# Performance work log

Measured on AMD Instinct MI355X. Metric: run time of the kernel, lower is better.

Reference implementation:

```python
import jax, jax.numpy as jnp
import numpy as np

N = 11616          # IMDB total nodes (hard-coded slices in source)
NHID = 512
L = 4              # num_layers (encoder and decoder each)
E = 371712         # ~32 avg degree
SIZES = [4278, 2081, 5257]
FEATS = [3066, 2081, 5257]
GAMMA = 3.0


def setup_inputs() -> dict:
    key = jax.random.key(0)
    ks = jax.random.split(key, 24)
    s = 0.02
    d = {}
    d["X0"] = jax.random.normal(ks[0], (SIZES[0], FEATS[0]), jnp.float32)
    d["X1"] = jax.random.normal(ks[1], (SIZES[1], FEATS[1]), jnp.float32)
    d["X2"] = jax.random.normal(ks[2], (SIZES[2], FEATS[2]), jnp.float32)
    d["src"] = jax.random.randint(ks[3], (E,), 0, N)
    d["dst"] = jax.random.randint(ks[4], (E,), 0, N)
    d["edge_w"] = jax.random.uniform(ks[5], (E,), jnp.float32) / 32.0  # ~normalized adjacency values
    d["adj_full"] = (jax.random.uniform(ks[6], (N, N), jnp.float32) < 0.005).astype(jnp.float32)
    # input projections fc_list: feat_dim -> nhid
    for i in range(3):
        d[f"fc_W{i}"] = jax.random.normal(ks[7 + i], (FEATS[i], NHID), jnp.float32) * s
        d[f"fc_b{i}"] = jnp.zeros((NHID,), jnp.float32)
    # stacked GraphConvolution weights (encoder / decoder)
    d["enc_W"] = jax.random.normal(ks[10], (L, NHID, NHID), jnp.float32) * s
    d["enc_b"] = jnp.zeros((L, NHID), jnp.float32)
    d["dec_W"] = jax.random.normal(ks[11], (L, NHID, NHID), jnp.float32) * s
    d["dec_b"] = jnp.zeros((L, NHID), jnp.float32)
    # output projections fc_list2: nhid -> feat_dim
    for i in range(3):
        d[f"out_W{i}"] = jax.random.normal(ks[12 + i], (NHID, FEATS[i]), jnp.float32) * s
        d[f"out_b{i}"] = jnp.zeros((FEATS[i],), jnp.float32)
    return d


def reference(X0, X1, X2, edge_w, adj_full,
              fc_W0, fc_b0, fc_W1, fc_b1, fc_W2, fc_b2,
              enc_W, enc_b, dec_W, dec_b,
              out_W0, out_b0, out_W1, out_b1, out_W2, out_b2,
              src, dst):
    def spmm(h):  # sparse A @ h via edge list
        return jax.ops.segment_sum(h[src] * edge_w[:, None], dst, num_segments=N)

    # per-type input projection, concat over node types -> [N, NHID]
    x = jnp.concatenate([X0 @ fc_W0 + fc_b0,
                         X1 @ fc_W1 + fc_b1,
                         X2 @ fc_W2 + fc_b2], axis=0)

    # encoder then decoder; per source: relu+dropout only at layer 0 (L>1 branch),
    # residual add for layers i>0; dropout is identity in eval mode.
    for W, b in ((enc_W, enc_b), (dec_W, dec_b)):
        for i in range(L):
            h = spmm(x @ W[i]) + b[i]
            x = jax.nn.relu(h) if i == 0 else x + h

    # IMDB slices of final embedding
    e0, e1, e2 = x[:SIZES[0]], x[SIZES[0]:SIZES[0] + SIZES[1]], x[SIZES[0] + SIZES[1]:]
    r0 = e0 @ out_W0 + out_b0
    r1 = e1 @ out_W1 + out_b1
    r2 = e2 @ out_W2 + out_b2

    # emb_loss_fun2: BCE(sigmoid(x x^T), adj_full), mean. Stable form:
    z = x @ x.T  # [N, N]
    emb_loss = jnp.mean(adj_full * jax.nn.softplus(-z) + (1.0 - adj_full) * jax.nn.softplus(z))

    # recon_loss_fun2 on type-0 features (cosine-based, power gamma)
    rn = r0 / jnp.maximum(jnp.linalg.norm(r0, axis=-1, keepdims=True), 1e-12)
    fn = X0 / jnp.maximum(jnp.linalg.norm(X0, axis=1, keepdims=True), 1e-12)
    recon_loss = jnp.mean((1.0 - jnp.sum(rn * fn, axis=-1)) ** GAMMA)

    return (r0, r1, r2, emb_loss, recon_loss)
```

## Files before the change

### kernel.cpp

```cpp
#include <hip/hip_runtime.h>
#include <math.h>

#define N_NODES 11616
#define NROWPAD 11776
#define NHID    512
#define EDGES   371712
#define S0 4278
#define S1 2081
#define S2 5257
#define F0 3066
#define F1 2081
#define F2 5257
#define NBLK 91
#define FC_KS 4
#define WPR 363

typedef __attribute__((ext_vector_type(8))) short bf16x8;
typedef __attribute__((ext_vector_type(4))) float f32x4;

#define GL2LDS(g, l) __builtin_amdgcn_global_load_lds(                         \
    (const __attribute__((address_space(1))) unsigned int*)(g),                \
    (__attribute__((address_space(3))) unsigned int*)(l), 16, 0, 0)

__device__ __forceinline__ int slot_of(int row, int kg)
{
    return row * 4 + (kg ^ ((row >> 1) & 3));
}

__global__ void k_init(double* __restrict__ accum, int* __restrict__ indeg,
                       int* __restrict__ cursor)
{
    int i = blockIdx.x * blockDim.x + threadIdx.x;
    if (i < 2) accum[i] = 0.0;
    if (i < N_NODES) { indeg[i] = 0; cursor[i] = 0; }
}

__global__ void k_padzero(short* __restrict__ xh, short* __restrict__ xl)
{
    int i = blockIdx.x * blockDim.x + threadIdx.x;
    const int base  = N_NODES * NHID;
    const int total = (NROWPAD - N_NODES) * NHID;
    if (i < total) { xh[base + i] = 0; xl[base + i] = 0; }
}

__global__ void k_adjbits(const float* __restrict__ adj, unsigned* __restrict__ bits)
{
    const long i = (long)blockIdx.x * 256 + threadIdx.x;
    const long total = (long)N_NODES * WPR;
    if (i >= total) return;
    const int r = (int)(i / WPR);
    const int w = (int)(i % WPR);
    const float4* rp = reinterpret_cast<const float4*>(adj + (long)r * N_NODES + w * 32);
    unsigned m = 0;
    #pragma unroll
    for (int j4 = 0; j4 < 8; ++j4) {
        float4 v = rp[j4];
        int b = j4 * 4;
        m |= (v.x != 0.f) ? (1u << b)       : 0u;
        m |= (v.y != 0.f) ? (1u << (b + 1)) : 0u;
        m |= (v.z != 0.f) ? (1u << (b + 2)) : 0u;
        m |= (v.w != 0.f) ? (1u << (b + 3)) : 0u;
    }
    bits[i] = m;
}

__global__ void k_count(const int* __restrict__ dst, int* __restrict__ indeg)
{
    int e = blockIdx.x * blockDim.x + threadIdx.x;
    if (e < EDGES) atomicAdd(&indeg[dst[e]], 1);
}

__global__ void k_scan(const int* __restrict__ indeg, int* __restrict__ rowptr)
{
    __shared__ int part[256];
    const int t = threadIdx.x;
    const int chunk = (N_NODES + 255) / 256;
    const int base = t * chunk;
    int s = 0;
    for (int i = 0; i < chunk; ++i) {
        int idx = base + i;
        if (idx < N_NODES) s += indeg[idx];
    }
    part[t] = s;
    __syncthreads();
    if (t == 0) for (int i = 1; i < 256; ++i) part[i] += part[i - 1];
    __syncthreads();
    int run = (t == 0) ? 0 : part[t - 1];
    for (int i = 0; i < chunk; ++i) {
        int idx = base + i;
        if (idx < N_NODES) { rowptr[idx] = run; run += indeg[idx]; }
    }
    if (t == 0) rowptr[N_NODES] = part[255];
}

__global__ void k_fill(const int* __restrict__ src, const int* __restrict__ dst,
                       const float* __restrict__ ew, const int* __restrict__ rowptr,
                       int* __restrict__ cursor, int* __restrict__ csrc,
                       float* __restrict__ cw)
{
    int e = blockIdx.x * blockDim.x + threadIdx.x;
    if (e >= EDGES) return;
    int d = dst[e];
    int pos = rowptr[d] + atomicAdd(&cursor[d], 1);
    csrc[pos] = src[e];
    cw[pos]   = ew[e];
}

__device__ __forceinline__ void split_bf16(float f, short& hi, short& lo)
{
    unsigned u  = __float_as_uint(f);
    unsigned hr = (u + 0x7FFFu + ((u >> 16) & 1u)) & 0xFFFF0000u;
    float    fh = __uint_as_float(hr);
    float    fl = f - fh;
    unsigned ul = __float_as_uint(fl);
    unsigned lr = ul + 0x7FFFu + ((ul >> 16) & 1u);
    hi = (short)(hr >> 16);
    lo = (short)(lr >> 16);
}

__global__ void k_splitpad(const float* __restrict__ in, short* __restrict__ oh,
                           short* __restrict__ ol, int R, int C, int Cpad)
{
    const int c = blockIdx.x * 256 + threadIdx.x;
    const int r = blockIdx.y;
    if (c >= Cpad) return;
    float f = (r < R && c < C) ? in[(long)r * C + c] : 0.f;
    short h, l;
    split_bf16(f, h, l);
    oh[(long)r * Cpad + c] = h;
    ol[(long)r * Cpad + c] = l;
}

__global__ void k_tsplit(const float* __restrict__ in, short* __restrict__ oh,
                         short* __restrict__ ol, int R, int C, int Rpad, int Cpad)
{
    __shared__ float tile[32][33];
    const int cb = blockIdx.x * 32, rb = blockIdx.y * 32;
    const int tx = threadIdx.x, ty = threadIdx.y;
    #pragma unroll
    for (int i = ty; i < 32; i += 8) {
        int r = rb + i, c = cb + tx;
        tile[i][tx] = (r < R && c < C) ? in[(long)r * C + c] : 0.f;
    }
    __syncthreads();
    #pragma unroll
    for (int i = ty; i < 32; i += 8) {
        int row = cb + i, col = rb + tx;
        if (row < Cpad && col < Rpad) {
            short h, l;
            split_bf16(tile[tx][i], h, l);
            oh[(long)row * Rpad + col] = h;
            ol[(long)row * Rpad + col] = l;
        }
    }
}

__device__ __forceinline__ void stage_gl(const short* __restrict__ src, int ldk,
                                         int k0, short* ldsPanel, int lane)
{
    #pragma unroll
    for (int i = 0; i < 8; ++i) {
        int ci  = i * 64 + lane;
        int row = ci >> 2;
        int kgs = (ci & 3) ^ ((row >> 1) & 3);
        const short* g = src + (long)row * ldk + k0 + kgs * 8;
        GL2LDS(g, (char*)ldsPanel + i * 1024);
    }
}

__global__ __launch_bounds__(256, 3)
void k_gemm_bb(const short* __restrict__ Agh, const short* __restrict__ Agl,
               const short* __restrict__ Bgh, const short* __restrict__ Bgl,
               const float* __restrict__ bias, float* __restrict__ C,
               int M, int NN, int Kpad, int ldk)
{
    __shared__ short P[4][4096];
    const int t = threadIdx.x, lane = t & 63, w = t >> 6;
    const int rowBase = blockIdx.y * 128, colBase = blockIdx.x * 128;
    const int wm = (w >> 1) * 64, wn = (w & 1) * 64;
    const int kg = lane >> 4, fr = lane & 15;

    const short* srcs[4] = { Agh + (long)rowBase * ldk, Agl + (long)rowBase * ldk,
                             Bgh + (long)colBase * ldk, Bgl + (long)colBase * ldk };
    const short* mySrc = srcs[w];

    int offA[4], offB[4];
    #pragma unroll
    for (int f = 0; f < 4; ++f) {
        int rA = wm + f * 16 + fr, rB = wn + f * 16 + fr;
        offA[f] = slot_of(rA, kg) * 8;
        offB[f] = slot_of(rB, kg) * 8;
    }

    f32x4 acc[4][4];
    #pragma unroll
    for (int i = 0; i < 4; ++i)
        #pragma unroll
        for (int j = 0; j < 4; ++j)
            acc[i][j] = (f32x4){0.f, 0.f, 0.f, 0.f};

    for (int k0 = 0; k0 < Kpad; k0 += 32) {
        stage_gl(mySrc, ldk, k0, &P[w][0], lane);
        __syncthreads();
        bf16x8 ah[4], al[4], bh[4], bl[4];
        #pragma unroll
        for (int f = 0; f < 4; ++f) {
            ah[f] = *(const bf16x8*)&P[0][offA[f]];
            al[f] = *(const bf16x8*)&P[1][offA[f]];
            bh[f] = *(const bf16x8*)&P[2][offB[f]];
            bl[f] = *(const bf16x8*)&P[3][offB[f]];
        }
        #pragma unroll
        for (int i = 0; i < 4; ++i)
            #pragma unroll
            for (int j = 0; j < 4; ++j) {
                acc[i][j] = __builtin_amdgcn_mfma_f32_16x16x32_bf16(ah[i], bh[j], acc[i][j], 0, 0, 0);
                acc[i][j] = __builtin_amdgcn_mfma_f32_16x16x32_bf16(ah[i], bl[j], acc[i][j], 0, 0, 0);
                acc[i][j] = __builtin_amdgcn_mfma_f32_16x16x32_bf16(al[i], bh[j], acc[i][j], 0, 0, 0);
            }
        __syncthreads();
    }

    #pragma unroll
    for (int i = 0; i < 4; ++i) {
        #pragma unroll
        for (int q = 0; q < 4; ++q) {
            int r = rowBase + wm + i * 16 + kg * 4 + q;
            if (r >= M) continue;
            #pragma unroll
            for (int j = 0; j < 4; ++j) {
                int c = colBase + wn + j * 16 + fr;
                if (c < NN)
                    C[(long)r * NN + c] = acc[i][j][q] + (bias ? bias[c] : 0.f);
            }
        }
    }
}

__global__ __launch_bounds__(256, 3)
void k_gemm_red(const short* __restrict__ Agh, const short* __restrict__ Agl,
                const short* __restrict__ Bgh, const short* __restrict__ Bgl,
                float* __restrict__ Cpart, int M, int ldk, int kChunk)
{
    __shared__ short P[4][4096];
    const int t = threadIdx.x, lane = t & 63, w = t >> 6;
    const int rowBase = blockIdx.y * 128, colBase = blockIdx.x * 128;
    const int z = blockIdx.z;
    const int wm = (w >> 1) * 64, wn = (w & 1) * 64;
    const int kg = lane >> 4, fr = lane & 15;

    const short* srcs[4] = { Agh + (long)rowBase * ldk, Agl + (long)rowBase * ldk,
                             Bgh + (long)colBase * ldk, Bgl + (long)colBase * ldk };
    const short* mySrc = srcs[w];

    int offA[4], offB[4];
    #pragma unroll
    for (int f = 0; f < 4; ++f) {
        int rA = wm + f * 16 + fr, rB = wn + f * 16 + fr;
        offA[f] = slot_of(rA, kg) * 8;
        offB[f] = slot_of(rB, kg) * 8;
    }

    f32x4 acc[4][4];
    #pragma unroll
    for (int i = 0; i < 4; ++i)
        #pragma unroll
        for (int j = 0; j < 4; ++j)
            acc[i][j] = (f32x4){0.f, 0.f, 0.f, 0.f};

    const int kEnd = z * kChunk + kChunk;
    for (int k0 = z * kChunk; k0 < kEnd; k0 += 32) {
        stage_gl(mySrc, ldk, k0, &P[w][0], lane);
        __syncthreads();
        bf16x8 ah[4], al[4], bh[4], bl[4];
        #pragma unroll
        for (int f = 0; f < 4; ++f) {
            ah[f] = *(const bf16x8*)&P[0][offA[f]];
            al[f] = *(const bf16x8*)&P[1][offA[f]];
            bh[f] = *(const bf16x8*)&P[2][offB[f]];
            bl[f] = *(const bf16x8*)&P[3][offB[f]];
        }
        #pragma unroll
        for (int i = 0; i < 4; ++i)
            #pragma unroll
            for (int j = 0; j < 4; ++j) {
                acc[i][j] = __builtin_amdgcn_mfma_f32_16x16x32_bf16(ah[i], bh[j], acc[i][j], 0, 0, 0);
                acc[i][j] = __builtin_amdgcn_mfma_f32_16x16x32_bf16(ah[i], bl[j], acc[i][j], 0, 0, 0);
                acc[i][j] = __builtin_amdgcn_mfma_f32_16x16x32_bf16(al[i], bh[j], acc[i][j], 0, 0, 0);
            }
        __syncthreads();
    }

    #pragma unroll
    for (int i = 0; i < 4; ++i) {
        #pragma unroll
        for (int q = 0; q < 4; ++q) {
            int r = rowBase + wm + i * 16 + kg * 4 + q;
            if (r >= M) continue;
            #pragma unroll
            for (int j = 0; j < 4; ++j) {
                int c = colBase + wn + j * 16 + fr;
                Cpart[((long)z * M + r) * NHID + c] = acc[i][j][q];
            }
        }
    }
}

__global__ void k_fcreduce(const float* __restrict__ Cpart, const float* __restrict__ bias,
                           int M, float* __restrict__ xo, short* __restrict__ oh,
                           short* __restrict__ ol)
{
    const int r = blockIdx.x;
    const int c = threadIdx.x << 2;
    float4 s = *reinterpret_cast<const float4*>(bias + c);
    #pragma unroll
    for (int z = 0; z < FC_KS; ++z) {
        const float4 p = *reinterpret_cast<const float4*>(Cpart + ((long)z * M + r) * NHID + c);
        s.x += p.x; s.y += p.y; s.z += p.z; s.w += p.w;
    }
    *reinterpret_cast<float4*>(xo + (long)r * NHID + c) = s;
    short4 h, l;
    split_bf16(s.x, h.x, l.x); split_bf16(s.y, h.y, l.y);
    split_bf16(s.z, h.z, l.z); split_bf16(s.w, h.w, l.w);
    *reinterpret_cast<short4*>(oh + (long)r * NHID + c) = h;
    *reinterpret_cast<short4*>(ol + (long)r * NHID + c) = l;
}

__global__ __launch_bounds__(256, 3)
void k_zloss(const short* __restrict__ xh, const short* __restrict__ xl,
             const unsigned* __restrict__ bits, double* __restrict__ accum)
{
    __shared__ short P[4][4096];
    __shared__ float ztr[4][16][17];
    __shared__ float red[256];
    const int t = threadIdx.x, lane = t & 63, w = t >> 6;

    int b = blockIdx.x, R = 0;
    while (b >= NBLK - R) { b -= NBLK - R; ++R; }
    const int Cb = R + b;
    const int rowBase = R * 128, colBase = Cb * 128;
    const int diag = (Cb == R);

    const int wm = (w >> 1) * 64, wn = (w & 1) * 64;
    const int kg = lane >> 4, fr = lane & 15;

    const short* srcs[4] = { xh + (long)rowBase * NHID, xl + (long)rowBase * NHID,
                             xh + (long)colBase * NHID, xl + (long)colBase * NHID };
    const short* mySrc = srcs[w];

    int offA[4], offB[4];
    #pragma unroll
    for (int f = 0; f < 4; ++f) {
        int rA = wm + f * 16 + fr, rB = wn + f * 16 + fr;
        offA[f] = slot_of(rA, kg) * 8;
        offB[f] = slot_of(rB, kg) * 8;
    }

    f32x4 acc[4][4];
    #pragma unroll
    for (int i = 0; i < 4; ++i)
        #pragma unroll
        for (int j = 0; j < 4; ++j)
            acc[i][j] = (f32x4){0.f, 0.f, 0.f, 0.f};

    for (int k0 = 0; k0 < NHID; k0 += 32) {
        stage_gl(mySrc, NHID, k0, &P[w][0], lane);
        __syncthreads();
        bf16x8 ah[4], al[4], bh[4], bl[4];
        #pragma unroll
        for (int f = 0; f < 4; ++f) {
            ah[f] = *(const bf16x8*)&P[0][offA[f]];
            al[f] = *(const bf16x8*)&P[1][offA[f]];
            bh[f] = *(const bf16x8*)&P[2][offB[f]];
            bl[f] = *(const bf16x8*)&P[3][offB[f]];
        }
        #pragma unroll
        for (int i = 0; i < 4; ++i)
            #pragma unroll
            for (int j = 0; j < 4; ++j) {
                acc[i][j] = __builtin_amdgcn_mfma_f32_16x16x32_bf16(ah[i], bh[j], acc[i][j], 0, 0, 0);
                acc[i][j] = __builtin_amdgcn_mfma_f32_16x16x32_bf16(ah[i], bl[j], acc[i][j], 0, 0, 0);
                acc[i][j] = __builtin_amdgcn_mfma_f32_16x16x32_bf16(al[i], bh[j], acc[i][j], 0, 0, 0);
            }
        __syncthreads();
    }

    float local = 0.f;
    #pragma unroll
    for (int i = 0; i < 4; ++i) {
        #pragma unroll
        for (int q = 0; q < 4; ++q) {
            int r = rowBase + wm + i * 16 + kg * 4 + q;
            if (r >= N_NODES) continue;
            #pragma unroll
            for (int j = 0; j < 4; ++j) {
                int c = colBase + wn + j * 16 + fr;
                if (c >= N_NODES) continue;
                float z  = acc[i][j][q];
                float sp = fmaxf(z, 0.f) + __logf(1.f + __expf(-fabsf(z)));
                unsigned wd = bits[(long)r * WPR + (c >> 5)];
                float az = ((wd >> (c & 31)) & 1u) ? z : 0.f;
                local += diag ? (sp - az) : (2.f * sp - az);
            }
        }
    }
    if (!diag) {
        #pragma unroll
        for (int i = 0; i < 4; ++i) {
            #pragma unroll
            for (int j = 0; j < 4; ++j) {
                #pragma unroll
                for (int q = 0; q < 4; ++q)
                    ztr[w][kg * 4 + q][fr] = acc[i][j][q];
                #pragma unroll
                for (int q = 0; q < 4; ++q) {
                    float zt = ztr[w][fr][kg * 4 + q];
                    int cc = colBase + wn + j * 16 + kg * 4 + q;
                    int rr = rowBase + wm + i * 16 + fr;
                    if (cc < N_NODES && rr < N_NODES) {
                        unsigned wd = bits[(long)cc * WPR + (rr >> 5)];
                        if ((wd >> (rr & 31)) & 1u) local -= zt;
                    }
                }
            }
        }
    }
    red[t] = local;
    __syncthreads();
    for (int sft = 128; sft > 0; sft >>= 1) {
        if (t < sft) red[t] += red[t + sft];
        __syncthreads();
    }
    if (t == 0) atomicAdd(accum, (double)red[0]);
}

__global__ void k_spmm(const float* __restrict__ y, const float* __restrict__ xold,
                       const int* __restrict__ rowptr, const int* __restrict__ csrc,
                       const float* __restrict__ cw, const float* __restrict__ bias,
                       int do_relu, float* __restrict__ xnew,
                       short* __restrict__ xh, short* __restrict__ xl)
{
    const int wv   = threadIdx.x >> 6;
    const int lane = threadIdx.x & 63;
    const int n    = blockIdx.x * 4 + wv;
    const int c1   = lane << 2;
    const int c2   = c1 + 256;
    float4 s1 = make_float4(0.f, 0.f, 0.f, 0.f);
    float4 s2 = make_float4(0.f, 0.f, 0.f, 0.f);
    const int beg = rowptr[n], end = rowptr[n + 1];
    for (int e = beg; e < end; ++e) {
        int   sn = csrc[e];
        float wt = cw[e];
        const float* yr = y + (long)sn * NHID;
        const float4 y1 = *reinterpret_cast<const float4*>(yr + c1);
        const float4 y2 = *reinterpret_cast<const float4*>(yr + c2);
        s1.x = fmaf(wt, y1.x, s1.x); s1.y = fmaf(wt, y1.y, s1.y);
        s1.z = fmaf(wt, y1.z, s1.z); s1.w = fmaf(wt, y1.w, s1.w);
        s2.x = fmaf(wt, y2.x, s2.x); s2.y = fmaf(wt, y2.y, s2.y);
        s2.z = fmaf(wt, y2.z, s2.z); s2.w = fmaf(wt, y2.w, s2.w);
    }
    const float4 b1 = *reinterpret_cast<const float4*>(bias + c1);
    const float4 b2 = *reinterpret_cast<const float4*>(bias + c2);
    float4 o1, o2;
    o1.x = s1.x + b1.x; o1.y = s1.y + b1.y; o1.z = s1.z + b1.z; o1.w = s1.w + b1.w;
    o2.x = s2.x + b2.x; o2.y = s2.y + b2.y; o2.z = s2.z + b2.z; o2.w = s2.w + b2.w;
    if (do_relu) {
        o1.x = fmaxf(o1.x, 0.f); o1.y = fmaxf(o1.y, 0.f);
        o1.z = fmaxf(o1.z, 0.f); o1.w = fmaxf(o1.w, 0.f);
        o2.x = fmaxf(o2.x, 0.f); o2.y = fmaxf(o2.y, 0.f);
        o2.z = fmaxf(o2.z, 0.f); o2.w = fmaxf(o2.w, 0.f);
    } else {
        const float4 x1 = *reinterpret_cast<const float4*>(xold + (long)n * NHID + c1);
        const float4 x2 = *reinterpret_cast<const float4*>(xold + (long)n * NHID + c2);
        o1.x += x1.x; o1.y += x1.y; o1.z += x1.z; o1.w += x1.w;
        o2.x += x2.x; o2.y += x2.y; o2.z += x2.z; o2.w += x2.w;
    }
    *reinterpret_cast<float4*>(xnew + (long)n * NHID + c1) = o1;
    *reinterpret_cast<float4*>(xnew + (long)n * NHID + c2) = o2;
    short4 h, l;
    split_bf16(o1.x, h.x, l.x); split_bf16(o1.y, h.y, l.y);
    split_bf16(o1.z, h.z, l.z); split_bf16(o1.w, h.w, l.w);
    *reinterpret_cast<short4*>(xh + (long)n * NHID + c1) = h;
    *reinterpret_cast<short4*>(xl + (long)n * NHID + c1) = l;
    split_bf16(o2.x, h.x, l.x); split_bf16(o2.y, h.y, l.y);
    split_bf16(o2.z, h.z, l.z); split_bf16(o2.w, h.w, l.w);
    *reinterpret_cast<short4*>(xh + (long)n * NHID + c2) = h;
    *reinterpret_cast<short4*>(xl + (long)n * NHID + c2) = l;
}

__global__ void k_recon(const float* __restrict__ r0, const float* __restrict__ X0,
                        double* __restrict__ accum)
{
    const int row = blockIdx.x;
    const int t = threadIdx.x;
    float dot = 0.f, nr = 0.f, nf = 0.f;
    for (int c = t; c < F0; c += 256) {
        float a = r0[(long)row * F0 + c];
        float b = X0[(long)row * F0 + c];
        dot = fmaf(a, b, dot);
        nr  = fmaf(a, a, nr);
        nf  = fmaf(b, b, nf);
    }
    #pragma unroll
    for (int o = 32; o > 0; o >>= 1) {
        dot += __shfl_down(dot, o);
        nr  += __shfl_down(nr, o);
        nf  += __shfl_down(nf, o);
    }
    __shared__ float sd[3][4];
    const int lane = t & 63, wid = t >> 6;
    if (lane == 0) { sd[0][wid] = dot; sd[1][wid] = nr; sd[2][wid] = nf; }
    __syncthreads();
    if (t == 0) {
        float d = sd[0][0] + sd[0][1] + sd[0][2] + sd[0][3];
        float a = sd[1][0] + sd[1][1] + sd[1][2] + sd[1][3];
        float b = sd[2][0] + sd[2][1] + sd[2][2] + sd[2][3];
        float cosv = d / (fmaxf(sqrtf(a), 1e-12f) * fmaxf(sqrtf(b), 1e-12f));
        float v = 1.f - cosv;
        atomicAdd(accum + 1, (double)(v * v * v));
    }
}

__global__ void k_final(const double* __restrict__ accum, float* __restrict__ out)
{
    if (threadIdx.x == 0) {
        out[45082958] = (float)(accum[0] / ((double)N_NODES * (double)N_NODES));
        out[45082959] = (float)(accum[1] / (double)S0);
    }
}

extern "C" void kernel_launch(void* const* d_in, const int* in_sizes, int n_in,
                              void* d_out, int out_size, void* d_ws, size_t ws_size,
                              hipStream_t stream)
{
    const float* X0  = (const float*)d_in[0];
    const float* X1  = (const float*)d_in[1];
    const float* X2  = (const float*)d_in[2];
    const int*   src = (const int*)d_in[3];
    const int*   dst = (const int*)d_in[4];
    const float* ew  = (const float*)d_in[5];
    const float* adj = (const float*)d_in[6];
    const float* fcW[3]  = {(const float*)d_in[7],  (const float*)d_in[9],  (const float*)d_in[11]};
    const float* fcB[3]  = {(const float*)d_in[8],  (const float*)d_in[10], (const float*)d_in[12]};
    const float* encW = (const float*)d_in[13];
    const float* encB = (const float*)d_in[14];
    const float* decW = (const float*)d_in[15];
    const float* decB = (const float*)d_in[16];
    const float* outW[3] = {(const float*)d_in[17], (const float*)d_in[19], (const float*)d_in[21]};
    const float* outB[3] = {(const float*)d_in[18], (const float*)d_in[20], (const float*)d_in[22]};
    float* out = (float*)d_out;

    const int FD[3]     = {F0, F1, F2};
    const int FPAD[3]   = {(F0 + 127) & ~127, (F1 + 127) & ~127, (F2 + 127) & ~127};
    const int SPAD[3]   = {(S0 + 127) & ~127, (S1 + 127) & ~127, (S2 + 127) & ~127};
    const int SD[3]     = {S0, S1, S2};
    const float* XD[3]  = {X0, X1, X2};

    char* ws = (char*)d_ws;
    size_t off = 0;
    auto alloc = [&](size_t bytes) { void* p = ws + off; off += (bytes + 255) & ~(size_t)255; return p; };

    double* accum = (double*)alloc(16);
    const size_t XB = (size_t)N_NODES * NHID * sizeof(float);
    float* xbuf = (float*)alloc(XB);
    float* ybuf = (float*)alloc(XB);
    float* xalt = (float*)alloc(XB);
    short* xh   = (short*)alloc((size_t)NROWPAD * NHID * 2);
    short* xl   = (short*)alloc((size_t)NROWPAD * NHID * 2);
    const size_t XSmax = (size_t)5376 * 5376;
    short* Xsh  = (short*)alloc(XSmax * 2);
    short* Xsl  = (short*)alloc(XSmax * 2);
    short* fcWh = (short*)alloc((size_t)NHID * 5376 * 2);
    short* fcWl = (short*)alloc((size_t)NHID * 5376 * 2);
    short* wTh  = (short*)alloc((size_t)8 * NHID * NHID * 2);
    short* wTl  = (short*)alloc((size_t)8 * NHID * NHID * 2);
    unsigned* bits = (unsigned*)alloc((size_t)N_NODES * WPR * 4);
    int* indeg  = (int*)alloc((size_t)N_NODES * 4);
    int* rowptr = (int*)alloc((size_t)(N_NODES + 1) * 4);
    int* cursor = (int*)alloc((size_t)N_NODES * 4);
    int* csrc   = (int*)alloc((size_t)EDGES * 4);
    float* cw   = (float*)alloc((size_t)EDGES * 4);

    float* cpart = ybuf;

    k_init<<<dim3((N_NODES + 255) / 256), dim3(256), 0, stream>>>(accum, indeg, cursor);
    k_padzero<<<dim3(((NROWPAD - N_NODES) * NHID + 255) / 256), dim3(256), 0, stream>>>(xh, xl);
    k_count<<<dim3((EDGES + 255) / 256), dim3(256), 0, stream>>>(dst, indeg);
    k_scan<<<dim3(1), dim3(256), 0, stream>>>(indeg, rowptr);
    k_fill<<<dim3((EDGES + 255) / 256), dim3(256), 0, stream>>>(src, dst, ew, rowptr, cursor, csrc, cw);
    {
        long words = (long)N_NODES * WPR;
        k_adjbits<<<dim3((unsigned)((words + 255) / 256)), dim3(256), 0, stream>>>(adj, bits);
    }

    auto tgrid = [](int Cpad, int Rpad) { return dim3((unsigned)((Cpad + 31) / 32), (unsigned)((Rpad + 31) / 32)); };
    auto ggrid = [](int m, int nn) { return dim3((unsigned)((nn + 127) / 128), (unsigned)((m + 127) / 128)); };

    for (int i = 0; i < 4; ++i) {
        k_tsplit<<<tgrid(NHID, NHID), dim3(32, 8), 0, stream>>>(
            encW + (size_t)i * NHID * NHID, wTh + (size_t)i * NHID * NHID,
            wTl + (size_t)i * NHID * NHID, NHID, NHID, NHID, NHID);
        k_tsplit<<<tgrid(NHID, NHID), dim3(32, 8), 0, stream>>>(
            decW + (size_t)i * NHID * NHID, wTh + (size_t)(4 + i) * NHID * NHID,
            wTl + (size_t)(4 + i) * NHID * NHID, NHID, NHID, NHID, NHID);
    }

    {
        size_t rowoff = 0;
        for (int i = 0; i < 3; ++i) {
            k_splitpad<<<dim3((FPAD[i] + 255) / 256, SPAD[i]), dim3(256), 0, stream>>>(
                XD[i], Xsh, Xsl, SD[i], FD[i], FPAD[i]);
            k_tsplit<<<tgrid(NHID, FPAD[i]), dim3(32, 8), 0, stream>>>(
                fcW[i], fcWh, fcWl, FD[i], NHID, FPAD[i], NHID);
            k_gemm_red<<<dim3(NHID / 128, SPAD[i] / 128, FC_KS), dim3(256), 0, stream>>>(
                Xsh, Xsl, fcWh, fcWl, cpart, SD[i], FPAD[i], FPAD[i] / FC_KS);
            k_fcreduce<<<dim3(SD[i]), dim3(128), 0, stream>>>(
                cpart, fcB[i], SD[i], xbuf + rowoff * NHID,
                xh + rowoff * NHID, xl + rowoff * NHID);
            rowoff += SD[i];
        }
    }

    float* x  = xbuf;
    float* xn = xalt;
    for (int phase = 0; phase < 2; ++phase) {
        const float* B = phase ? decB : encB;
        for (int i = 0; i < 4; ++i) {
            k_gemm_bb<<<ggrid(N_NODES, NHID), dim3(256), 0, stream>>>(
                xh, xl, wTh + (size_t)(phase * 4 + i) * NHID * NHID,
                wTl + (size_t)(phase * 4 + i) * NHID * NHID,
                nullptr, ybuf, N_NODES, NHID, NHID, NHID);
            k_spmm<<<dim3(N_NODES / 4), dim3(256), 0, stream>>>(
                ybuf, x, rowptr, csrc, cw, B + (size_t)i * NHID, (i == 0) ? 1 : 0,
                xn, xh, xl);
            float* tmp = x; x = xn; xn = tmp;
        }
    }

    short* oWh = Xsh;
    short* oWl = Xsl;
    {
        short *ph = oWh, *pl = oWl;
        for (int i = 0; i < 3; ++i) {
            int FDP = (FD[i] + 127) & ~127;
            k_tsplit<<<tgrid(FDP, NHID), dim3(32, 8), 0, stream>>>(
                outW[i], ph, pl, NHID, FD[i], NHID, FDP);
            ph += (size_t)FDP * NHID; pl += (size_t)FDP * NHID;
        }
    }

    {
        short *ph = oWh, *pl = oWl;
        float* oo = out;
        size_t rowoff = 0;
        for (int i = 0; i < 3; ++i) {
            int FDP = (FD[i] + 127) & ~127;
            k_gemm_bb<<<ggrid(SD[i], FD[i]), dim3(256), 0, stream>>>(
                xh + rowoff * NHID, xl + rowoff * NHID, ph, pl, outB[i], oo,
                SD[i], FD[i], NHID, NHID);
            ph += (size_t)FDP * NHID; pl += (size_t)FDP * NHID;
            oo += (size_t)SD[i] * FD[i];
            rowoff += SD[i];
        }
    }

    k_zloss<<<dim3(NBLK * (NBLK + 1) / 2), dim3(256), 0, stream>>>(xh, xl, bits, accum);
    k_recon<<<dim3(S0), dim3(256), 0, stream>>>(out, X0, accum);
    k_final<<<dim3(1), dim3(64), 0, stream>>>(accum, out);
}
```

Measured before the change: 2.291 ms.

## Drop fp32 activation copy, split spmm rows across waves, remap zloss blocks per XCD

The fp32 activation buffer is removed. The residual in k_spmm is now rebuilt from the bf16 hi/lo split arrays, so the fp32 write and read of x per layer go away. k_spmm now gives each wave half a row, doubling the grid for more parallelism at the cost of re-reading the CSR indices twice. k_zloss maps block IDs so that each XCD handles contiguous 4x4 super-tile bands of the triangle, aiming for better L2 reuse of row and column tiles. The residual reconstructed from hi+lo is close to but not bit-identical with the fp32 value.

```diff
diff --git a/kernel.cpp b/kernel.cpp
--- a/kernel.cpp
+++ b/kernel.cpp
@@ -12,6 +12,7 @@
 #define F1 2081
 #define F2 5257
 #define NBLK 91
+#define NZBLK 4186
 #define FC_KS 4
 #define WPR 363
 
@@ -25,6 +26,11 @@
 __device__ __forceinline__ int slot_of(int row, int kg)
 {
     return row * 4 + (kg ^ ((row >> 1) & 3));
+}
+
+__device__ __forceinline__ float bf2f(short s)
+{
+    return __uint_as_float(((unsigned)(unsigned short)s) << 16);
 }
 
 __global__ void k_init(double* __restrict__ accum, int* __restrict__ indeg,
@@ -307,8 +313,7 @@
 }
 
 __global__ void k_fcreduce(const float* __restrict__ Cpart, const float* __restrict__ bias,
-                           int M, float* __restrict__ xo, short* __restrict__ oh,
-                           short* __restrict__ ol)
+                           int M, short* __restrict__ oh, short* __restrict__ ol)
 {
     const int r = blockIdx.x;
     const int c = threadIdx.x << 2;
@@ -318,7 +323,6 @@
         const float4 p = *reinterpret_cast<const float4*>(Cpart + ((long)z * M + r) * NHID + c);
         s.x += p.x; s.y += p.y; s.z += p.z; s.w += p.w;
     }
-    *reinterpret_cast<float4*>(xo + (long)r * NHID + c) = s;
     short4 h, l;
     split_bf16(s.x, h.x, l.x); split_bf16(s.y, h.y, l.y);
     split_bf16(s.z, h.z, l.z); split_bf16(s.w, h.w, l.w);
@@ -335,9 +339,43 @@
     __shared__ float red[256];
     const int t = threadIdx.x, lane = t & 63, w = t >> 6;
 
-    int b = blockIdx.x, R = 0;
-    while (b >= NBLK - R) { b -= NBLK - R; ++R; }
-    const int Cb = R + b;
+    int L;
+    {
+        const int q = NZBLK / 8, rr = NZBLK % 8;
+        int d = blockIdx.x;
+        int xcd = d & 7, pos = d >> 3;
+        L = (xcd < rr) ? xcd * (q + 1) + pos : rr * (q + 1) + (xcd - rr) * q + pos;
+    }
+    int R, Cb;
+    {
+        int RS = 0;
+        for (;;) {
+            int nr  = min(4, NBLK - RS * 4);
+            int tri = nr * (nr + 1) / 2;
+            int rest = NBLK - (RS + 1) * 4;
+            if (rest < 0) rest = 0;
+            int band = tri + nr * rest;
+            if (L < band) break;
+            L -= band; ++RS;
+        }
+        int nr  = min(4, NBLK - RS * 4);
+        int tri = nr * (nr + 1) / 2;
+        if (L < tri) {
+            int r = 0;
+            while (L >= nr - r) { L -= nr - r; ++r; }
+            R  = RS * 4 + r;
+            Cb = RS * 4 + r + L;
+        } else {
+            L -= tri;
+            int CS = RS + 1;
+            for (;;) {
+                int nc  = min(4, NBLK - CS * 4);
+                int cnt = nr * nc;
+                if (L < cnt) { R = RS * 4 + L / nc; Cb = CS * 4 + L % nc; break; }
+                L -= cnt; ++CS;
+            }
+        }
+    }
     const int rowBase = R * 128, colBase = Cb * 128;
     const int diag = (Cb == R);
 
@@ -434,58 +472,45 @@
     if (t == 0) atomicAdd(accum, (double)red[0]);
 }
 
-__global__ void k_spmm(const float* __restrict__ y, const float* __restrict__ xold,
+__global__ void k_spmm(const float* __restrict__ y,
                        const int* __restrict__ rowptr, const int* __restrict__ csrc,
                        const float* __restrict__ cw, const float* __restrict__ bias,
-                       int do_relu, float* __restrict__ xnew,
-                       short* __restrict__ xh, short* __restrict__ xl)
+                       int do_relu, short* __restrict__ xh, short* __restrict__ xl)
 {
     const int wv   = threadIdx.x >> 6;
     const int lane = threadIdx.x & 63;
-    const int n    = blockIdx.x * 4 + wv;
-    const int c1   = lane << 2;
-    const int c2   = c1 + 256;
-    float4 s1 = make_float4(0.f, 0.f, 0.f, 0.f);
-    float4 s2 = make_float4(0.f, 0.f, 0.f, 0.f);
+    const int n    = blockIdx.x * 2 + (wv >> 1);
+    const int c    = (wv & 1) * 256 + (lane << 2);
+    float4 s = make_float4(0.f, 0.f, 0.f, 0.f);
     const int beg = rowptr[n], end = rowptr[n + 1];
     for (int e = beg; e < end; ++e) {
         int   sn = csrc[e];
         float wt = cw[e];
-        const float* yr = y + (long)sn * NHID;
-        const float4 y1 = *reinterpret_cast<const float4*>(yr + c1);
-        const float4 y2 = *reinterpret_cast<const float4*>(yr + c2);
-        s1.x = fmaf(wt, y1.x, s1.x); s1.y = fmaf(wt, y1.y, s1.y);
-        s1.z = fmaf(wt, y1.z, s1.z); s1.w = fmaf(wt, y1.w, s1.w);
-        s2.x = fmaf(wt, y2.x, s2.x); s2.y = fmaf(wt, y2.y, s2.y);
-        s2.z = fmaf(wt, y2.z, s2.z); s2.w = fmaf(wt, y2.w, s2.w);
-    }
-    const float4 b1 = *reinterpret_cast<const float4*>(bias + c1);
-    const float4 b2 = *reinterpret_cast<const float4*>(bias + c2);
-    float4 o1, o2;
-    o1.x = s1.x + b1.x; o1.y = s1.y + b1.y; o1.z = s1.z + b1.z; o1.w = s1.w + b1.w;
-    o2.x = s2.x + b2.x; o2.y = s2.y + b2.y; o2.z = s2.z + b2.z; o2.w = s2.w + b2.w;
+        const float4 yv = *reinterpret_cast<const float4*>(y + (long)sn * NHID + c);
+        s.x = fmaf(wt, yv.x, s.x);
+        s.y = fmaf(wt, yv.y, s.y);
+        s.z = fmaf(wt, yv.z, s.z);
+        s.w = fmaf(wt, yv.w, s.w);
+    }
+    const float4 bv = *reinterpret_cast<const float4*>(bias + c);
+    float4 o;
+    o.x = s.x + bv.x; o.y = s.y + bv.y; o.z = s.z + bv.z; o.w = s.w + bv.w;
     if (do_relu) {
-        o1.x = fmaxf(o1.x, 0.f); o1.y = fmaxf(o1.y, 0.f);
-        o1.z = fmaxf(o1.z, 0.f); o1.w = fmaxf(o1.w, 0.f);
-        o2.x = fmaxf(o2.x, 0.f); o2.y = fmaxf(o2.y, 0.f);
-        o2.z = fmaxf(o2.z, 0.f); o2.w = fmaxf(o2.w, 0.f);
+        o.x = fmaxf(o.x, 0.f); o.y = fmaxf(o.y, 0.f);
+        o.z = fmaxf(o.z, 0.f); o.w = fmaxf(o.w, 0.f);
     } else {
-        const float4 x1 = *reinterpret_cast<const float4*>(xold + (long)n * NHID + c1);
-        const float4 x2 = *reinterpret_cast<const float4*>(xold + (long)n * NHID + c2);
-        o1.x += x1.x; o1.y += x1.y; o1.z += x1.z; o1.w += x1.w;
-        o2.x += x2.x; o2.y += x2.y; o2.z += x2.z; o2.w += x2.w;
-    }
-    *reinterpret_cast<float4*>(xnew + (long)n * NHID + c1) = o1;
-    *reinterpret_cast<float4*>(xnew + (long)n * NHID + c2) = o2;
+        const short4 h4 = *reinterpret_cast<const short4*>(xh + (long)n * NHID + c);
+        const short4 l4 = *reinterpret_cast<const short4*>(xl + (long)n * NHID + c);
+        o.x += bf2f(h4.x) + bf2f(l4.x);
+        o.y += bf2f(h4.y) + bf2f(l4.y);
+        o.z += bf2f(h4.z) + bf2f(l4.z);
+        o.w += bf2f(h4.w) + bf2f(l4.w);
+    }
     short4 h, l;
-    split_bf16(o1.x, h.x, l.x); split_bf16(o1.y, h.y, l.y);
-    split_bf16(o1.z, h.z, l.z); split_bf16(o1.w, h.w, l.w);
-    *reinterpret_cast<short4*>(xh + (long)n * NHID + c1) = h;
-    *reinterpret_cast<short4*>(xl + (long)n * NHID + c1) = l;
-    split_bf16(o2.x, h.x, l.x); split_bf16(o2.y, h.y, l.y);
-    split_bf16(o2.z, h.z, l.z); split_bf16(o2.w, h.w, l.w);
-    *reinterpret_cast<short4*>(xh + (long)n * NHID + c2) = h;
-    *reinterpret_cast<short4*>(xl + (long)n * NHID + c2) = l;
+    split_bf16(o.x, h.x, l.x); split_bf16(o.y, h.y, l.y);
+    split_bf16(o.z, h.z, l.z); split_bf16(o.w, h.w, l.w);
+    *reinterpret_cast<short4*>(xh + (long)n * NHID + c) = h;
+    *reinterpret_cast<short4*>(xl + (long)n * NHID + c) = l;
 }
 
 __global__ void k_recon(const float* __restrict__ r0, const float* __restrict__ X0,
@@ -562,7 +587,6 @@
 
     double* accum = (double*)alloc(16);
     const size_t XB = (size_t)N_NODES * NHID * sizeof(float);
-    float* xbuf = (float*)alloc(XB);
     float* ybuf = (float*)alloc(XB);
     float* xalt = (float*)alloc(XB);
     short* xh   = (short*)alloc((size_t)NROWPAD * NHID * 2);
@@ -615,14 +639,11 @@
             k_gemm_red<<<dim3(NHID / 128, SPAD[i] / 128, FC_KS), dim3(256), 0, stream>>>(
                 Xsh, Xsl, fcWh, fcWl, cpart, SD[i], FPAD[i], FPAD[i] / FC_KS);
             k_fcreduce<<<dim3(SD[i]), dim3(128), 0, stream>>>(
-                cpart, fcB[i], SD[i], xbuf + rowoff * NHID,
-                xh + rowoff * NHID, xl + rowoff * NHID);
+                cpart, fcB[i], SD[i], xh + rowoff * NHID, xl + rowoff * NHID);
             rowoff += SD[i];
         }
     }
 
-    float* x  = xbuf;
-    float* xn = xalt;
     for (int phase = 0; phase < 2; ++phase) {
         const float* B = phase ? decB : encB;
         for (int i = 0; i < 4; ++i) {
@@ -630,10 +651,9 @@
                 xh, xl, wTh + (size_t)(phase * 4 + i) * NHID * NHID,
                 wTl + (size_t)(phase * 4 + i) * NHID * NHID,
                 nullptr, ybuf, N_NODES, NHID, NHID, NHID);
-            k_spmm<<<dim3(N_NODES / 4), dim3(256), 0, stream>>>(
-                ybuf, x, rowptr, csrc, cw, B + (size_t)i * NHID, (i == 0) ? 1 : 0,
-                xn, xh, xl);
-            float* tmp = x; x = xn; xn = tmp;
+            k_spmm<<<dim3(N_NODES / 2), dim3(256), 0, stream>>>(
+                ybuf, rowptr, csrc, cw, B + (size_t)i * NHID, (i == 0) ? 1 : 0,
+                xh, xl);
         }
     }
 
@@ -664,7 +684,7 @@
         }
     }
 
-    k_zloss<<<dim3(NBLK * (NBLK + 1) / 2), dim3(256), 0, stream>>>(xh, xl, bits, accum);
+    k_zloss<<<dim3(NZBLK), dim3(256), 0, stream>>>(xh, xl, bits, accum);
     k_recon<<<dim3(S0), dim3(256), 0, stream>>>(out, X0, accum);
     k_final<<<dim3(1), dim3(64), 0, stream>>>(accum, out);
 }
```

Result: no change. 2.254 ms (median of 2 runs) (-1.6%).
